# Optimization experiments

Measured on AMD Instinct MI355X. Metric: run time of the kernel, lower is better.

## Reference

```python
import jax, jax.numpy as jnp
import numpy as np

H, W, C = 768, 768, 64


def _segment_ids(mask):
    """mask: [L] int binary separator mask -> [L] int32 segment ids.
    A new grid segment starts at each rising edge (0 -> 1) of the mask;
    pixel 0 always belongs to segment 0. Equivalent to GridStructureBuilder's
    run-based row/column partition, derived via a single cumsum."""
    m = mask.astype(jnp.int32)
    prev = jnp.concatenate([jnp.zeros((1,), jnp.int32), m[:-1]])
    rising = ((m == 1) & (prev == 0)).at[0].set(False)
    return jnp.cumsum(rising.astype(jnp.int32))


def setup_inputs() -> dict:
    key = jax.random.key(0)
    k1, k2, k3 = jax.random.split(key, 3)
    return {
        "input": jax.random.normal(k1, (1, H, W, C), dtype=jnp.float32),
        "h_mask": jax.random.randint(k2, (1, H), 0, 2, dtype=jnp.int32),
        "v_mask": jax.random.randint(k3, (1, W), 0, 2, dtype=jnp.int32),
    }


def reference(input, h_mask, v_mask):
    x = input[0]                      # [H, W, C]
    h, w, c = x.shape
    row_ids = _segment_ids(h_mask[0])  # [H]
    col_ids = _segment_ids(v_mask[0])  # [W]
    # flat cell id per pixel; w is a static upper bound on the column count
    idx = (row_ids[:, None] * w + col_ids[None, :]).reshape(-1)  # [H*W]
    xf = x.reshape(h * w, c)
    n_seg = h * w                      # static upper bound on cell count
    sums = jax.ops.segment_sum(xf, idx, num_segments=n_seg)           # [n_seg, C]
    counts = jax.ops.segment_sum(jnp.ones((h * w,), x.dtype), idx,
                                 num_segments=n_seg)                  # [n_seg]
    # scatter-add of (1/area)*x == per-cell mean
    means = sums / jnp.maximum(counts, 1.0)[:, None]
    # keep_size=True: gather cell means back to every pixel
    return means[idx].reshape(1, h, w, c)
```

## Files before the change

### kernel.cpp

```cpp
#include <hip/hip_runtime.h>


#define GH 768
#define GW 768
#define MAXSEG 385
#define ROWQ (GW * 16)

enum {
    OFF_ROWSTART = 0,
    OFF_ROWEND   = OFF_ROWSTART + MAXSEG,
    OFF_COLSTART = OFF_ROWEND + MAXSEG,
    OFF_COLEND   = OFF_COLSTART + MAXSEG,
    OFF_NROWS    = OFF_COLEND + MAXSEG,
    OFF_NCOLS,
    OFF_RID,
    OFF_CID = OFF_RID + GH,
    OFF_END = OFF_CID + GW,
};

#define COLSUM_OFF_BYTES  16384
#define COLSUM_CAP_BYTES  ((size_t)MAXSEG * ROWQ * 16)
#define MEANS_OFF_BYTES   (COLSUM_OFF_BYTES + COLSUM_CAP_BYTES)
#define MEANS_CAP_BYTES   ((size_t)MAXSEG * MAXSEG * 16 * 16)
#define WS_NEED_BYTES     (MEANS_OFF_BYTES + MEANS_CAP_BYTES)

__device__ __forceinline__ void acc4(float4& a, const float4 v) {
    a.x += v.x; a.y += v.y; a.z += v.z; a.w += v.w;
}

__global__ __launch_bounds__(768) void seg_scan(const int* __restrict__ h_mask,
                                                const int* __restrict__ v_mask,
                                                int* __restrict__ ws) {
    __shared__ int s[GH];
    const int i = threadIdx.x;
    const bool is_row = (blockIdx.x == 0);
    const int* m = is_row ? h_mask : v_mask;

    int rising = 0;
    if (i > 0) rising = (m[i] == 1 && m[i - 1] == 0) ? 1 : 0;
    s[i] = rising;
    __syncthreads();

    for (int off = 1; off < GH; off <<= 1) {
        int add = (i >= off) ? s[i - off] : 0;
        __syncthreads();
        s[i] += add;
        __syncthreads();
    }

    const int seg  = s[i];
    const int segL = (i == 0)      ? -1 : s[i - 1];
    const int segR = (i == GH - 1) ? -2 : s[i + 1];

    int* start = ws + (is_row ? OFF_ROWSTART : OFF_COLSTART);
    int* end   = ws + (is_row ? OFF_ROWEND   : OFF_COLEND);
    if (seg != segL) start[seg] = i;
    if (seg != segR) end[seg]   = i + 1;
    ws[(is_row ? OFF_RID : OFF_CID) + i] = seg;
    if (i == GH - 1) ws[is_row ? OFF_NROWS : OFF_NCOLS] = seg + 1;
}

__global__ __launch_bounds__(256) void col_sum(const float4* __restrict__ in,
                                               float4* __restrict__ colsum,
                                               const int* __restrict__ ws) {
    const int N = ws[OFF_NROWS] * ROWQ;
    const int stride = gridDim.x * blockDim.x;
    for (int u = blockIdx.x * blockDim.x + threadIdx.x; u < N; u += stride) {
        const int r   = u / ROWQ;
        const int rem = u - r * ROWQ;
        const int y0 = ws[OFF_ROWSTART + r];
        const int y1 = ws[OFF_ROWEND + r];
        float4 a0 = make_float4(0.f,0.f,0.f,0.f), a1 = a0, a2 = a0, a3 = a0;
        int y = y0;
        for (; y + 3 < y1; y += 4) {
            acc4(a0, in[(size_t)y * ROWQ + rem]);
            acc4(a1, in[(size_t)(y + 1) * ROWQ + rem]);
            acc4(a2, in[(size_t)(y + 2) * ROWQ + rem]);
            acc4(a3, in[(size_t)(y + 3) * ROWQ + rem]);
        }
        for (; y < y1; ++y) acc4(a0, in[(size_t)y * ROWQ + rem]);
        acc4(a0, a1); acc4(a2, a3); acc4(a0, a2);
        colsum[u] = a0;
    }
}

__global__ __launch_bounds__(256) void cell_mean(const float4* __restrict__ colsum,
                                                 float4* __restrict__ means,
                                                 const int* __restrict__ ws) {
    const int nrows = ws[OFF_NROWS];
    const int ncols = ws[OFF_NCOLS];
    const int N = nrows * ncols * 16;
    const int stride = gridDim.x * blockDim.x;
    for (int v = blockIdx.x * blockDim.x + threadIdx.x; v < N; v += stride) {
        const int cq = v & 15;
        const int rs = v >> 4;
        const int r  = rs / ncols;
        const int s  = rs - r * ncols;
        const int x0 = ws[OFF_COLSTART + s];
        const int x1 = ws[OFF_COLEND + s];
        float4 a = make_float4(0.f,0.f,0.f,0.f);
        for (int x = x0; x < x1; ++x)
            acc4(a, colsum[(size_t)r * ROWQ + x * 16 + cq]);
        const float area =
            (float)((ws[OFF_ROWEND + r] - ws[OFF_ROWSTART + r]) * (x1 - x0));
        means[v] = make_float4(a.x / area, a.y / area, a.z / area, a.w / area);
    }
}

__global__ __launch_bounds__(256) void bcast(const float4* __restrict__ means,
                                             float4* __restrict__ out,
                                             const int* __restrict__ ws) {
    __shared__ int scid[GW];
    const int y   = blockIdx.x;
    const int tid = threadIdx.x;
    for (int x = tid; x < GW; x += 256) scid[x] = ws[OFF_CID + x];
    const int rid   = ws[OFF_RID + y];
    const int ncols = ws[OFF_NCOLS];
    const size_t mrow = (size_t)rid * ncols * 16;
    __syncthreads();

    float4* orow = out + (size_t)y * ROWQ;
    #pragma unroll 4
    for (int u = tid; u < ROWQ; u += 256) {
        const int x  = u >> 4;
        const int cq = u & 15;
        orow[u] = means[mrow + (size_t)scid[x] * 16 + cq];
    }
}

__global__ __launch_bounds__(256) void cell_pool(const float4* __restrict__ in,
                                                 float4* __restrict__ out,
                                                 const int* __restrict__ ws) {
    const int nrows  = ws[OFF_NROWS];
    const int ncols  = ws[OFF_NCOLS];
    const int ncells = nrows * ncols;
    const int wave   = blockIdx.x * 4 + (threadIdx.x >> 6);
    const int nwaves = gridDim.x * 4;
    const int lane   = threadIdx.x & 63;
    const int pg     = lane >> 4;
    const int cq     = lane & 15;

    for (int cell = wave; cell < ncells; cell += nwaves) {
        const int br = cell / ncols;
        const int bc = cell - br * ncols;
        const int y0 = ws[OFF_ROWSTART + br];
        const int y1 = ws[OFF_ROWEND + br];
        const int x0 = ws[OFF_COLSTART + bc];
        const int x1 = ws[OFF_COLEND + bc];
        float4 a = make_float4(0.f,0.f,0.f,0.f);
        for (int y = y0; y < y1; ++y) {
            const size_t rb = (size_t)y * ROWQ + cq;
            for (int x = x0 + pg; x < x1; x += 4)
                acc4(a, in[rb + (size_t)x * 16]);
        }
        #pragma unroll
        for (int msk = 16; msk < 64; msk <<= 1) {
            a.x += __shfl_xor(a.x, msk, 64);
            a.y += __shfl_xor(a.y, msk, 64);
            a.z += __shfl_xor(a.z, msk, 64);
            a.w += __shfl_xor(a.w, msk, 64);
        }
        const float area = (float)((y1 - y0) * (x1 - x0));
        float4 mn = make_float4(a.x / area, a.y / area, a.z / area, a.w / area);
        for (int y = y0; y < y1; ++y) {
            const size_t rb = (size_t)y * ROWQ + cq;
            for (int x = x0 + pg; x < x1; x += 4)
                out[rb + (size_t)x * 16] = mn;
        }
    }
}

extern "C" void kernel_launch(void* const* d_in, const int* in_sizes, int n_in,
                              void* d_out, int out_size, void* d_ws, size_t ws_size,
                              hipStream_t stream) {
    const float* in  = (const float*)d_in[0];
    const int* hmask = (const int*)d_in[1];
    const int* vmask = (const int*)d_in[2];
    float* out = (float*)d_out;
    int* ws = (int*)d_ws;

    seg_scan<<<2, GH, 0, stream>>>(hmask, vmask, ws);

    if (ws_size >= WS_NEED_BYTES) {
        float4* colsum = (float4*)((char*)d_ws + COLSUM_OFF_BYTES);
        float4* means  = (float4*)((char*)d_ws + MEANS_OFF_BYTES);
        col_sum<<<4096, 256, 0, stream>>>((const float4*)in, colsum, ws);
        cell_mean<<<2048, 256, 0, stream>>>(colsum, means, ws);
        bcast<<<GH, 256, 0, stream>>>(means, (float4*)out, ws);
    } else {
        cell_pool<<<2048, 256, 0, stream>>>((const float4*)in, (float4*)out, ws);
    }
}
```

Measured before the change: 297.3 us.

## Replace colsum/cell_mean passes with tiled shared-memory pooling and atomic accumulation

Drops the global column-sum intermediate and the separate cell-mean pass. Each 8x32 pixel tile now sums rows within a segment into shared memory, reduces across column segments, and atomically adds partial sums into a zeroed means buffer. A finalize pass then scales by precomputed inverse areas. This removes a large global write and read of colsum, but adds a zeroing pass, float atomics, and extra kernel launches.

After: 299.2 us. No clear change (+0.6%).

```diff
diff --git a/kernel.cpp b/kernel.cpp
--- a/kernel.cpp
+++ b/kernel.cpp
@@ -5,6 +5,8 @@
 #define GW 768
 #define MAXSEG 385
 #define ROWQ (GW * 16)
+#define TH 8
+#define TW 32
 
 enum {
     OFF_ROWSTART = 0,
@@ -18,11 +20,10 @@
     OFF_END = OFF_CID + GW,
 };
 
-#define COLSUM_OFF_BYTES  16384
-#define COLSUM_CAP_BYTES  ((size_t)MAXSEG * ROWQ * 16)
-#define MEANS_OFF_BYTES   (COLSUM_OFF_BYTES + COLSUM_CAP_BYTES)
-#define MEANS_CAP_BYTES   ((size_t)MAXSEG * MAXSEG * 16 * 16)
-#define WS_NEED_BYTES     (MEANS_OFF_BYTES + MEANS_CAP_BYTES)
+#define MEANS_OFF_BYTES 16384
+#define MEANS_CAP_F4    ((size_t)MAXSEG * MAXSEG * 16)
+#define INV_OFF_BYTES   (MEANS_OFF_BYTES + MEANS_CAP_F4 * 16)
+#define WS_NEED_BYTES   (INV_OFF_BYTES + (size_t)MAXSEG * MAXSEG * 4)
 
 __device__ __forceinline__ void acc4(float4& a, const float4 v) {
     a.x += v.x; a.y += v.y; a.z += v.z; a.w += v.w;
@@ -60,71 +61,110 @@
     if (i == GH - 1) ws[is_row ? OFF_NROWS : OFF_NCOLS] = seg + 1;
 }
 
-__global__ __launch_bounds__(256) void col_sum(const float4* __restrict__ in,
-                                               float4* __restrict__ colsum,
-                                               const int* __restrict__ ws) {
-    const int N = ws[OFF_NROWS] * ROWQ;
+__global__ __launch_bounds__(256) void prep(float4* __restrict__ means,
+                                            float* __restrict__ inv,
+                                            const int* __restrict__ ws) {
+    const int nrows = ws[OFF_NROWS];
+    const int ncols = ws[OFF_NCOLS];
+    const int ncells = nrows * ncols;
     const int stride = gridDim.x * blockDim.x;
-    for (int u = blockIdx.x * blockDim.x + threadIdx.x; u < N; u += stride) {
-        const int r   = u / ROWQ;
-        const int rem = u - r * ROWQ;
-        const int y0 = ws[OFF_ROWSTART + r];
-        const int y1 = ws[OFF_ROWEND + r];
-        float4 a0 = make_float4(0.f,0.f,0.f,0.f), a1 = a0, a2 = a0, a3 = a0;
-        int y = y0;
-        for (; y + 3 < y1; y += 4) {
-            acc4(a0, in[(size_t)y * ROWQ + rem]);
-            acc4(a1, in[(size_t)(y + 1) * ROWQ + rem]);
-            acc4(a2, in[(size_t)(y + 2) * ROWQ + rem]);
-            acc4(a3, in[(size_t)(y + 3) * ROWQ + rem]);
-        }
-        for (; y < y1; ++y) acc4(a0, in[(size_t)y * ROWQ + rem]);
-        acc4(a0, a1); acc4(a2, a3); acc4(a0, a2);
-        colsum[u] = a0;
-    }
-}
-
-__global__ __launch_bounds__(256) void cell_mean(const float4* __restrict__ colsum,
+    const float4 z = make_float4(0.f, 0.f, 0.f, 0.f);
+    for (int v = blockIdx.x * blockDim.x + threadIdx.x; v < ncells * 16; v += stride)
+        means[v] = z;
+    for (int v = blockIdx.x * blockDim.x + threadIdx.x; v < ncells; v += stride) {
+        const int r = v / ncols;
+        const int s = v - r * ncols;
+        const int h = ws[OFF_ROWEND + r] - ws[OFF_ROWSTART + r];
+        const int w = ws[OFF_COLEND + s] - ws[OFF_COLSTART + s];
+        inv[v] = 1.0f / (float)(h * w);
+    }
+}
+
+__global__ __launch_bounds__(256) void tile_pool(const float4* __restrict__ in,
                                                  float4* __restrict__ means,
                                                  const int* __restrict__ ws) {
-    const int nrows = ws[OFF_NROWS];
-    const int ncols = ws[OFF_NCOLS];
-    const int N = nrows * ncols * 16;
+    const int tx0 = blockIdx.x * TW;
+    const int ty0 = blockIdx.y * TH;
+    const int tid = threadIdx.x;
+
+    __shared__ int scid[TW];
+    __shared__ int srid[TH];
+    __shared__ float4 colsum[TW * 16];
+
+    if (tid < TW) scid[tid] = ws[OFF_CID + tx0 + tid];
+    if (tid < TH) srid[tid] = ws[OFF_RID + ty0 + tid];
+    __syncthreads();
+
+    const int ncols   = ws[OFF_NCOLS];
+    const int s_first = scid[0];
+    const int s_last  = scid[TW - 1];
+    const int nst     = s_last - s_first + 1;
+
+    const int u0 = tid, u1 = tid + 256;
+
+    int y = 0;
+    while (y < TH) {
+        const int r = srid[y];
+        int ye = y + 1;
+        while (ye < TH && srid[ye] == r) ++ye;
+
+        float4 a0 = make_float4(0.f,0.f,0.f,0.f), a1 = a0;
+        for (int yy = y; yy < ye; ++yy) {
+            const size_t base = ((size_t)(ty0 + yy) * GW + tx0) * 16;
+            acc4(a0, in[base + u0]);
+            acc4(a1, in[base + u1]);
+        }
+        colsum[u0] = a0;
+        colsum[u1] = a1;
+        __syncthreads();
+
+        for (int v = tid; v < nst * 16; v += 256) {
+            const int sl = v >> 4, cq = v & 15;
+            const int sg = s_first + sl;
+            int gx0 = ws[OFF_COLSTART + sg] - tx0; if (gx0 < 0) gx0 = 0;
+            int gx1 = ws[OFF_COLEND + sg]   - tx0; if (gx1 > TW) gx1 = TW;
+            float4 a = make_float4(0.f,0.f,0.f,0.f);
+            for (int x = gx0; x < gx1; ++x) acc4(a, colsum[x * 16 + cq]);
+            float* dst = (float*)&means[((size_t)r * ncols + sg) * 16 + cq];
+            unsafeAtomicAdd(dst + 0, a.x);
+            unsafeAtomicAdd(dst + 1, a.y);
+            unsafeAtomicAdd(dst + 2, a.z);
+            unsafeAtomicAdd(dst + 3, a.w);
+        }
+        __syncthreads();
+        y = ye;
+    }
+}
+
+__global__ __launch_bounds__(256) void finalize(float4* __restrict__ means,
+                                                const float* __restrict__ inv,
+                                                const int* __restrict__ ws) {
+    const int ncells = ws[OFF_NROWS] * ws[OFF_NCOLS];
     const int stride = gridDim.x * blockDim.x;
-    for (int v = blockIdx.x * blockDim.x + threadIdx.x; v < N; v += stride) {
-        const int cq = v & 15;
-        const int rs = v >> 4;
-        const int r  = rs / ncols;
-        const int s  = rs - r * ncols;
-        const int x0 = ws[OFF_COLSTART + s];
-        const int x1 = ws[OFF_COLEND + s];
-        float4 a = make_float4(0.f,0.f,0.f,0.f);
-        for (int x = x0; x < x1; ++x)
-            acc4(a, colsum[(size_t)r * ROWQ + x * 16 + cq]);
-        const float area =
-            (float)((ws[OFF_ROWEND + r] - ws[OFF_ROWSTART + r]) * (x1 - x0));
-        means[v] = make_float4(a.x / area, a.y / area, a.z / area, a.w / area);
+    for (int v = blockIdx.x * blockDim.x + threadIdx.x; v < ncells * 16; v += stride) {
+        const float s = inv[v >> 4];
+        float4 m = means[v];
+        m.x *= s; m.y *= s; m.z *= s; m.w *= s;
+        means[v] = m;
     }
 }
 
 __global__ __launch_bounds__(256) void bcast(const float4* __restrict__ means,
                                              float4* __restrict__ out,
                                              const int* __restrict__ ws) {
-    __shared__ int scid[GW];
+    __shared__ int scell[GW];
     const int y   = blockIdx.x;
     const int tid = threadIdx.x;
-    for (int x = tid; x < GW; x += 256) scid[x] = ws[OFF_CID + x];
     const int rid   = ws[OFF_RID + y];
     const int ncols = ws[OFF_NCOLS];
-    const size_t mrow = (size_t)rid * ncols * 16;
+    for (int x = tid; x < GW; x += 256)
+        scell[x] = rid * ncols + ws[OFF_CID + x];
     __syncthreads();
 
     float4* orow = out + (size_t)y * ROWQ;
     #pragma unroll 4
     for (int u = tid; u < ROWQ; u += 256) {
-        const int x  = u >> 4;
-        const int cq = u & 15;
-        orow[u] = means[mrow + (size_t)scid[x] * 16 + cq];
+        orow[u] = means[(size_t)scell[u >> 4] * 16 + (u & 15)];
     }
 }
 
@@ -148,8 +188,8 @@
         const int x0 = ws[OFF_COLSTART + bc];
         const int x1 = ws[OFF_COLEND + bc];
         float4 a = make_float4(0.f,0.f,0.f,0.f);
-        for (int y = y0; y < y1; ++y) {
-            const size_t rb = (size_t)y * ROWQ + cq;
+        for (int yy = y0; yy < y1; ++yy) {
+            const size_t rb = (size_t)yy * ROWQ + cq;
             for (int x = x0 + pg; x < x1; x += 4)
                 acc4(a, in[rb + (size_t)x * 16]);
         }
@@ -162,8 +202,8 @@
         }
         const float area = (float)((y1 - y0) * (x1 - x0));
         float4 mn = make_float4(a.x / area, a.y / area, a.z / area, a.w / area);
-        for (int y = y0; y < y1; ++y) {
-            const size_t rb = (size_t)y * ROWQ + cq;
+        for (int yy = y0; yy < y1; ++yy) {
+            const size_t rb = (size_t)yy * ROWQ + cq;
             for (int x = x0 + pg; x < x1; x += 4)
                 out[rb + (size_t)x * 16] = mn;
         }
@@ -182,10 +222,12 @@
     seg_scan<<<2, GH, 0, stream>>>(hmask, vmask, ws);
 
     if (ws_size >= WS_NEED_BYTES) {
-        float4* colsum = (float4*)((char*)d_ws + COLSUM_OFF_BYTES);
-        float4* means  = (float4*)((char*)d_ws + MEANS_OFF_BYTES);
-        col_sum<<<4096, 256, 0, stream>>>((const float4*)in, colsum, ws);
-        cell_mean<<<2048, 256, 0, stream>>>(colsum, means, ws);
+        float4* means = (float4*)((char*)d_ws + MEANS_OFF_BYTES);
+        float* inv    = (float*)((char*)d_ws + INV_OFF_BYTES);
+        prep<<<1024, 256, 0, stream>>>(means, inv, ws);
+        dim3 tg(GW / TW, GH / TH);
+        tile_pool<<<tg, 256, 0, stream>>>((const float4*)in, means, ws);
+        finalize<<<512, 256, 0, stream>>>(means, inv, ws);
         bcast<<<GH, 256, 0, stream>>>(means, (float4*)out, ws);
     } else {
         cell_pool<<<2048, 256, 0, stream>>>((const float4*)in, (float4*)out, ws);
```
